# Kernel optimization log

Measured on AMD Instinct MI355X. Metric: run time of the kernel, lower is better.

## Reference

```python
import jax, jax.numpy as jnp
import numpy as np

GROUP_SIZE = 32
PACKED_SIZE = GROUP_SIZE * 3 // 8  # 12
OUT_FEATURES = 4096
IN_FEATURES = 4096

# Precomputed static unpack constants per position i in [0, 32)
_I = np.arange(GROUP_SIZE)
_BYTE_IDX = (_I * 3) // 8                     # which byte holds the low bits
_BIT_OFF = (_I * 3) % 8                       # bit offset inside that byte
_LOW_MASK = np.where(_BIT_OFF <= 5, 7, (1 << (8 - _BIT_OFF)) - 1)
_HIGH_MASK = np.where(_BIT_OFF <= 5, 0, (1 << np.maximum(_BIT_OFF - 5, 0)) - 1)
_HIGH_SHIFT = np.where(_BIT_OFF <= 5, 0, 8 - _BIT_OFF)
_BYTE_IDX_NEXT = np.minimum(_BYTE_IDX + 1, PACKED_SIZE - 1)


def block_dequantize_3bit(packed, normalization):
    """packed: [G, 12] int (uint8 values), normalization: [G, 1] -> [G*32] f32."""
    p = packed.astype(jnp.int32)
    norm = normalization.astype(jnp.float32)
    b0 = p[:, _BYTE_IDX]        # [G, 32]
    b1 = p[:, _BYTE_IDX_NEXT]   # [G, 32]
    shift = jnp.asarray(_BIT_OFF, jnp.int32)
    low = (b0 >> shift) & jnp.asarray(_LOW_MASK, jnp.int32)
    high = (b1 & jnp.asarray(_HIGH_MASK, jnp.int32)) << jnp.asarray(_HIGH_SHIFT, jnp.int32)
    x_quant = (low | high).astype(jnp.float32)  # values in [0, 7]
    x_norm = x_quant / 7.0
    x = x_norm * 2.0 * norm - norm              # [G, 32]
    return x.reshape(-1)


def setup_inputs() -> dict:
    key = jax.random.key(0)
    k1, k2, k3, k4 = jax.random.split(key, 4)
    num_groups = OUT_FEATURES * IN_FEATURES // GROUP_SIZE
    x = jax.random.normal(k1, (8192, IN_FEATURES), dtype=jnp.float32)
    weight_q3 = jax.random.randint(k2, (num_groups, PACKED_SIZE), 0, 256, dtype=jnp.int32).astype(jnp.uint8)
    weight_norm = (jax.random.uniform(k3, (num_groups, 1), dtype=jnp.float32) * 0.99 + 0.01).astype(jnp.float16)
    bias = (jax.random.normal(k4, (OUT_FEATURES,), dtype=jnp.float32) * 0.02).astype(jnp.float16)
    return {"x": x, "weight_q3": weight_q3, "weight_norm": weight_norm, "bias": bias}


def reference(x, weight_q3, weight_norm, bias):
    w_flat = block_dequantize_3bit(weight_q3, weight_norm)          # f32 [out*in]
    w = w_flat.reshape(OUT_FEATURES, IN_FEATURES).astype(jnp.float16)
    x_half = x.astype(jnp.float16)
    result = jnp.dot(x_half, w.T) + bias                             # [N, out] fp16
    return result.astype(x.dtype)
```

## Files before the change

### kernel.cpp

```cpp
#include <hip/hip_runtime.h>
#include <hip/hip_fp16.h>
#include <stdint.h>

#define IN_F   4096
#define OUT_F  4096
#define M_ROWS 8192

typedef _Float16 v8h __attribute__((ext_vector_type(8)));
typedef float    v4f __attribute__((ext_vector_type(4)));

__global__ void __launch_bounds__(256)
prep_kernel(const int* __restrict__ q, const float* __restrict__ norm,
            _Float16* __restrict__ w, const float* __restrict__ x,
            _Float16* __restrict__ xo) {
    int blk = blockIdx.x;
    if (blk < 2048) {
        int g = blk * 256 + threadIdx.x;
        const int4* p = (const int4*)(q + (size_t)g * 12);
        int4 q0 = p[0], q1 = p[1], q2 = p[2];
        uint32_t b[12] = {(uint32_t)q0.x, (uint32_t)q0.y, (uint32_t)q0.z, (uint32_t)q0.w,
                          (uint32_t)q1.x, (uint32_t)q1.y, (uint32_t)q1.z, (uint32_t)q1.w,
                          (uint32_t)q2.x, (uint32_t)q2.y, (uint32_t)q2.z, (uint32_t)q2.w};
        uint64_t lo = 0, hi = 0;
#pragma unroll
        for (int i = 0; i < 8; ++i) lo |= (uint64_t)(b[i] & 0xff) << (8 * i);
#pragma unroll
        for (int i = 0; i < 8; ++i) hi |= (uint64_t)(b[4 + i] & 0xff) << (8 * i);
        float nrm = norm[g];
        float scale = nrm * (2.0f / 7.0f);
        v8h out[4];
#pragma unroll
        for (int i = 0; i < 32; ++i) {
            int p3 = 3 * i;
            uint32_t qv = (i <= 20) ? (uint32_t)((lo >> p3) & 7)
                                    : (uint32_t)((hi >> (p3 - 32)) & 7);
            float v = fmaf((float)qv, scale, -nrm);
            out[i >> 3][i & 7] = (_Float16)v;
        }
        v8h* dst = (v8h*)(w + (size_t)g * 32);
        dst[0] = out[0]; dst[1] = out[1]; dst[2] = out[2]; dst[3] = out[3];
    } else {
        size_t i = ((size_t)(blk - 2048) * 256 + threadIdx.x) * 8;
        float4 a = *(const float4*)(x + i);
        float4 c = *(const float4*)(x + i + 4);
        v8h r;
        r[0] = (_Float16)a.x; r[1] = (_Float16)a.y; r[2] = (_Float16)a.z; r[3] = (_Float16)a.w;
        r[4] = (_Float16)c.x; r[5] = (_Float16)c.y; r[6] = (_Float16)c.z; r[7] = (_Float16)c.w;
        *(v8h*)(xo + i) = r;
    }
}

#define KU 32

__global__ void __launch_bounds__(512, 2)
gemm_kernel(const _Float16* __restrict__ A,
            const _Float16* __restrict__ B,
            const float* __restrict__ bias,
            float* __restrict__ C) {
    __shared__ __align__(16) char smem[131072];

    int pid = blockIdx.x;
    int c  = pid & 7;
    int s  = pid >> 3;
    int pm = ((c & 3) << 3) | (s & 7);
    int pn = ((c >> 2) << 3) | (s >> 3);
    const int m0 = pm * 256, n0 = pn * 256;

    int t = threadIdx.x;
    int lane = t & 63, wid = t >> 6;
    int wm = wid >> 2, wn = wid & 3;
    int lr = lane & 15, qd = lane >> 4;

    int chr  = (((lane & 1) << 2) | qd) ^ ((lr >> 1) & 7);
    int aoff = wm * 8192 + (lr >> 1) * 128 + chr * 16;
    int boff = 16384 + wn * 4096 + (lr >> 1) * 128 + chr * 16;

    int line = t >> 3, chl = t & 7;
    int chd  = chl ^ (line & 7);
    int rr0  = 2 * line + (chd >> 2);
    int cc0  = chd & 3;
    const _Float16* gA0 = A + (size_t)(m0 + rr0) * IN_F + cc0 * 8;
    const _Float16* gA1 = gA0 + (size_t)128 * IN_F;
    const _Float16* gB0 = B + (size_t)(n0 + rr0) * IN_F + cc0 * 8;
    const _Float16* gB1 = gB0 + (size_t)128 * IN_F;
    const int dA = t * 16;
    const int dB = 16384 + t * 16;

    v4f acc[8][4] = {};

#define STAGE4(SL2)                                                                 \
    do {                                                                            \
        char* db_ = smem + (SL2) * 32768;                                           \
        __builtin_amdgcn_global_load_lds(                                           \
            (const __attribute__((address_space(1))) void*)gA0,                     \
            (__attribute__((address_space(3))) void*)(db_ + dA), 16, 0, 0);         \
        __builtin_amdgcn_global_load_lds(                                           \
            (const __attribute__((address_space(1))) void*)gA1,                     \
            (__attribute__((address_space(3))) void*)(db_ + dA + 8192), 16, 0, 0);  \
        __builtin_amdgcn_global_load_lds(                                           \
            (const __attribute__((address_space(1))) void*)gB0,                     \
            (__attribute__((address_space(3))) void*)(db_ + dB), 16, 0, 0);         \
        __builtin_amdgcn_global_load_lds(                                           \
            (const __attribute__((address_space(1))) void*)gB1,                     \
            (__attribute__((address_space(3))) void*)(db_ + dB + 8192), 16, 0, 0);  \
    } while (0)

#define STEP(SL, DO_STAGE, VM)                                                      \
    do {                                                                            \
        asm volatile("" ::: "memory");    \
        const char* slb = smem + (SL) * 32768;                                      \
        v8h a0_[4], a1_[4], bb_[4];                                                 \
        _Pragma("unroll") for (int i = 0; i < 4; ++i)                               \
            a0_[i] = *(const v8h*)(slb + aoff + i * 1024);                          \
        _Pragma("unroll") for (int j = 0; j < 4; ++j)                               \
            bb_[j] = *(const v8h*)(slb + boff + j * 1024);                          \
        _Pragma("unroll") for (int i = 0; i < 4; ++i)                               \
            a1_[i] = *(const v8h*)(slb + aoff + (i + 4) * 1024);                    \
        if (DO_STAGE) {                                                             \
            STAGE4((((SL) + 3) & 3));                                               \
            gA0 += KU; gA1 += KU; gB0 += KU; gB1 += KU;                             \
        }                                                                           \
        __builtin_amdgcn_s_setprio(1);                                              \
        _Pragma("unroll") for (int i = 0; i < 4; ++i)                               \
            _Pragma("unroll") for (int j = 0; j < 4; ++j)                           \
                acc[i][j] = __builtin_amdgcn_mfma_f32_16x16x32_f16(                 \
                    a0_[i], bb_[j], acc[i][j], 0, 0, 0);                            \
        _Pragma("unroll") for (int i = 0; i < 4; ++i)                               \
            _Pragma("unroll") for (int j = 0; j < 4; ++j)                           \
                acc[i + 4][j] = __builtin_amdgcn_mfma_f32_16x16x32_f16(             \
                    a1_[i], bb_[j], acc[i + 4][j], 0, 0, 0);                        \
        __builtin_amdgcn_s_setprio(0);                                              \
        asm volatile("s_waitcnt vmcnt(" #VM ")" ::: "memory");                      \
        __builtin_amdgcn_s_barrier();                                               \
    } while (0)

    STAGE4(0); gA0 += KU; gA1 += KU; gB0 += KU; gB1 += KU;
    STAGE4(1); gA0 += KU; gA1 += KU; gB0 += KU; gB1 += KU;
    STAGE4(2); gA0 += KU; gA1 += KU; gB0 += KU; gB1 += KU;
    asm volatile("s_waitcnt vmcnt(8)" ::: "memory");
    __builtin_amdgcn_s_barrier();

#pragma unroll 1
    for (int b4 = 0; b4 < 31; ++b4) {
        STEP(0, 1, 8);
        STEP(1, 1, 8);
        STEP(2, 1, 8);
        STEP(3, 1, 8);
    }
    STEP(0, 1, 8);
    STEP(1, 0, 4);
    STEP(2, 0, 0);
    STEP(3, 0, 0);
#undef STEP
#undef STAGE4

#pragma unroll
    for (int j = 0; j < 4; ++j) {
        int n = n0 + wn * 64 + j * 16 + lr;
        float bf = bias[n];
#pragma unroll
        for (int i = 0; i < 8; ++i) {
            int m = m0 + wm * 128 + i * 16 + qd * 4;
#pragma unroll
            for (int rr = 0; rr < 4; ++rr)
                C[(size_t)(m + rr) * OUT_F + n] = acc[i][j][rr] + bf;
        }
    }
}

extern "C" void kernel_launch(void* const* d_in, const int* in_sizes, int n_in,
                              void* d_out, int out_size, void* d_ws, size_t ws_size,
                              hipStream_t stream) {
    (void)in_sizes; (void)n_in; (void)out_size; (void)ws_size;
    const float* x    = (const float*)d_in[0];
    const int*   wq   = (const int*)d_in[1];
    const float* wnrm = (const float*)d_in[2];
    const float* bias = (const float*)d_in[3];
    float* out = (float*)d_out;

    _Float16* w16 = (_Float16*)d_ws;
    _Float16* x16 = (_Float16*)((char*)d_ws + (size_t)OUT_F * IN_F * 2);

    prep_kernel<<<2048 + 16384, 256, 0, stream>>>(wq, wnrm, w16, x, x16);

    int grid = (M_ROWS / 256) * (OUT_F / 256);
    gemm_kernel<<<grid, 512, 0, stream>>>(x16, w16, bias, out);
}
```

Before: 499.6 us.

## Double-buffer LDS fragment reads in registers and split prep kernel in two

The GEMM main loop now reads the next k-slice's A/B fragments from LDS into a second register set while MFMAs run on the current set, so LDS read latency overlaps compute. The vmcnt waits are tightened to match the earlier consumption of staged tiles. The fused prep kernel is also split into separate dequant and cast kernels, which adds one launch. The extra 48 fragment registers raise VGPR pressure at 2 waves per SIMD and could force spills.

Result: no change. 499.1 us (-0.1%).

```diff
diff --git a/kernel.cpp b/kernel.cpp
--- a/kernel.cpp
+++ b/kernel.cpp
@@ -10,44 +10,43 @@
 typedef float    v4f __attribute__((ext_vector_type(4)));
 
 __global__ void __launch_bounds__(256)
-prep_kernel(const int* __restrict__ q, const float* __restrict__ norm,
-            _Float16* __restrict__ w, const float* __restrict__ x,
-            _Float16* __restrict__ xo) {
-    int blk = blockIdx.x;
-    if (blk < 2048) {
-        int g = blk * 256 + threadIdx.x;
-        const int4* p = (const int4*)(q + (size_t)g * 12);
-        int4 q0 = p[0], q1 = p[1], q2 = p[2];
-        uint32_t b[12] = {(uint32_t)q0.x, (uint32_t)q0.y, (uint32_t)q0.z, (uint32_t)q0.w,
-                          (uint32_t)q1.x, (uint32_t)q1.y, (uint32_t)q1.z, (uint32_t)q1.w,
-                          (uint32_t)q2.x, (uint32_t)q2.y, (uint32_t)q2.z, (uint32_t)q2.w};
-        uint64_t lo = 0, hi = 0;
+dequant_kernel(const int* __restrict__ q, const float* __restrict__ norm,
+               _Float16* __restrict__ w) {
+    int g = blockIdx.x * blockDim.x + threadIdx.x;
+    const int4* p = (const int4*)(q + (size_t)g * 12);
+    int4 q0 = p[0], q1 = p[1], q2 = p[2];
+    uint32_t b[12] = {(uint32_t)q0.x, (uint32_t)q0.y, (uint32_t)q0.z, (uint32_t)q0.w,
+                      (uint32_t)q1.x, (uint32_t)q1.y, (uint32_t)q1.z, (uint32_t)q1.w,
+                      (uint32_t)q2.x, (uint32_t)q2.y, (uint32_t)q2.z, (uint32_t)q2.w};
+    uint64_t lo = 0, hi = 0;
 #pragma unroll
-        for (int i = 0; i < 8; ++i) lo |= (uint64_t)(b[i] & 0xff) << (8 * i);
+    for (int i = 0; i < 8; ++i) lo |= (uint64_t)(b[i] & 0xff) << (8 * i);
 #pragma unroll
-        for (int i = 0; i < 8; ++i) hi |= (uint64_t)(b[4 + i] & 0xff) << (8 * i);
-        float nrm = norm[g];
-        float scale = nrm * (2.0f / 7.0f);
-        v8h out[4];
+    for (int i = 0; i < 8; ++i) hi |= (uint64_t)(b[4 + i] & 0xff) << (8 * i);
+    float nrm = norm[g];
+    float scale = nrm * (2.0f / 7.0f);
+    v8h out[4];
 #pragma unroll
-        for (int i = 0; i < 32; ++i) {
-            int p3 = 3 * i;
-            uint32_t qv = (i <= 20) ? (uint32_t)((lo >> p3) & 7)
-                                    : (uint32_t)((hi >> (p3 - 32)) & 7);
-            float v = fmaf((float)qv, scale, -nrm);
-            out[i >> 3][i & 7] = (_Float16)v;
-        }
-        v8h* dst = (v8h*)(w + (size_t)g * 32);
-        dst[0] = out[0]; dst[1] = out[1]; dst[2] = out[2]; dst[3] = out[3];
-    } else {
-        size_t i = ((size_t)(blk - 2048) * 256 + threadIdx.x) * 8;
-        float4 a = *(const float4*)(x + i);
-        float4 c = *(const float4*)(x + i + 4);
-        v8h r;
-        r[0] = (_Float16)a.x; r[1] = (_Float16)a.y; r[2] = (_Float16)a.z; r[3] = (_Float16)a.w;
-        r[4] = (_Float16)c.x; r[5] = (_Float16)c.y; r[6] = (_Float16)c.z; r[7] = (_Float16)c.w;
-        *(v8h*)(xo + i) = r;
+    for (int i = 0; i < 32; ++i) {
+        int p3 = 3 * i;
+        uint32_t qv = (i <= 20) ? (uint32_t)((lo >> p3) & 7)
+                                : (uint32_t)((hi >> (p3 - 32)) & 7);
+        float v = fmaf((float)qv, scale, -nrm);
+        out[i >> 3][i & 7] = (_Float16)v;
     }
+    v8h* dst = (v8h*)(w + (size_t)g * 32);
+    dst[0] = out[0]; dst[1] = out[1]; dst[2] = out[2]; dst[3] = out[3];
+}
+
+__global__ void __launch_bounds__(256)
+castx_kernel(const float* __restrict__ x, _Float16* __restrict__ o) {
+    size_t i = ((size_t)blockIdx.x * blockDim.x + threadIdx.x) * 8;
+    float4 a = *(const float4*)(x + i);
+    float4 b = *(const float4*)(x + i + 4);
+    v8h r;
+    r[0] = (_Float16)a.x; r[1] = (_Float16)a.y; r[2] = (_Float16)a.z; r[3] = (_Float16)a.w;
+    r[4] = (_Float16)b.x; r[5] = (_Float16)b.y; r[6] = (_Float16)b.z; r[7] = (_Float16)b.w;
+    *(v8h*)(o + i) = r;
 }
 
 #define KU 32
@@ -87,6 +86,7 @@
     const int dB = 16384 + t * 16;
 
     v4f acc[8][4] = {};
+    v8h fa0[8], fb0[4], fa1[8], fb1[4];
 
 #define STAGE4(SL2)                                                                 \
     do {                                                                            \
@@ -105,30 +105,28 @@
             (__attribute__((address_space(3))) void*)(db_ + dB + 8192), 16, 0, 0);  \
     } while (0)
 
-#define STEP(SL, DO_STAGE, VM)                                                      \
+#define READFRAG(SLOT, FA, FB)                                                      \
     do {                                                                            \
-        asm volatile("" ::: "memory");    \
-        const char* slb = smem + (SL) * 32768;                                      \
-        v8h a0_[4], a1_[4], bb_[4];                                                 \
-        _Pragma("unroll") for (int i = 0; i < 4; ++i)                               \
-            a0_[i] = *(const v8h*)(slb + aoff + i * 1024);                          \
+        const char* sp_ = smem + (SLOT) * 32768;                                    \
+        _Pragma("unroll") for (int i = 0; i < 8; ++i)                               \
+            FA[i] = *(const v8h*)(sp_ + aoff + i * 1024);                           \
         _Pragma("unroll") for (int j = 0; j < 4; ++j)                               \
-            bb_[j] = *(const v8h*)(slb + boff + j * 1024);                          \
-        _Pragma("unroll") for (int i = 0; i < 4; ++i)                               \
-            a1_[i] = *(const v8h*)(slb + aoff + (i + 4) * 1024);                    \
+            FB[j] = *(const v8h*)(sp_ + boff + j * 1024);                           \
+    } while (0)
+
+#define STEP(SL, FCA, FCB, FNA, FNB, DO_STAGE, DO_PREF, VM)                         \
+    do {                                                                            \
+        asm volatile("" ::: "memory");      \
+        if (DO_PREF) READFRAG(((SL) + 1) & 3, FNA, FNB);                            \
         if (DO_STAGE) {                                                             \
-            STAGE4((((SL) + 3) & 3));                                               \
+            STAGE4(((SL) + 3) & 3);                                                 \
             gA0 += KU; gA1 += KU; gB0 += KU; gB1 += KU;                             \
         }                                                                           \
         __builtin_amdgcn_s_setprio(1);                                              \
-        _Pragma("unroll") for (int i = 0; i < 4; ++i)                               \
+        _Pragma("unroll") for (int i = 0; i < 8; ++i)                               \
             _Pragma("unroll") for (int j = 0; j < 4; ++j)                           \
                 acc[i][j] = __builtin_amdgcn_mfma_f32_16x16x32_f16(                 \
-                    a0_[i], bb_[j], acc[i][j], 0, 0, 0);                            \
-        _Pragma("unroll") for (int i = 0; i < 4; ++i)                               \
-            _Pragma("unroll") for (int j = 0; j < 4; ++j)                           \
-                acc[i + 4][j] = __builtin_amdgcn_mfma_f32_16x16x32_f16(             \
-                    a1_[i], bb_[j], acc[i + 4][j], 0, 0, 0);                        \
+                    FCA[i], FCB[j], acc[i][j], 0, 0, 0);                            \
         __builtin_amdgcn_s_setprio(0);                                              \
         asm volatile("s_waitcnt vmcnt(" #VM ")" ::: "memory");                      \
         __builtin_amdgcn_s_barrier();                                               \
@@ -137,21 +135,24 @@
     STAGE4(0); gA0 += KU; gA1 += KU; gB0 += KU; gB1 += KU;
     STAGE4(1); gA0 += KU; gA1 += KU; gB0 += KU; gB1 += KU;
     STAGE4(2); gA0 += KU; gA1 += KU; gB0 += KU; gB1 += KU;
-    asm volatile("s_waitcnt vmcnt(8)" ::: "memory");
+    asm volatile("s_waitcnt vmcnt(4)" ::: "memory");
     __builtin_amdgcn_s_barrier();
+    asm volatile("" ::: "memory");
+    READFRAG(0, fa0, fb0);
 
 #pragma unroll 1
     for (int b4 = 0; b4 < 31; ++b4) {
-        STEP(0, 1, 8);
-        STEP(1, 1, 8);
-        STEP(2, 1, 8);
-        STEP(3, 1, 8);
+        STEP(0, fa0, fb0, fa1, fb1, 1, 1, 4);
+        STEP(1, fa1, fb1, fa0, fb0, 1, 1, 4);
+        STEP(2, fa0, fb0, fa1, fb1, 1, 1, 4);
+        STEP(3, fa1, fb1, fa0, fb0, 1, 1, 4);
     }
-    STEP(0, 1, 8);
-    STEP(1, 0, 4);
-    STEP(2, 0, 0);
-    STEP(3, 0, 0);
+    STEP(0, fa0, fb0, fa1, fb1, 1, 1, 4);
+    STEP(1, fa1, fb1, fa0, fb0, 0, 1, 0);
+    STEP(2, fa0, fb0, fa1, fb1, 0, 1, 0);
+    STEP(3, fa1, fb1, fa0, fb0, 0, 0, 0);
 #undef STEP
+#undef READFRAG
 #undef STAGE4
 
 #pragma unroll
@@ -181,7 +182,9 @@
     _Float16* w16 = (_Float16*)d_ws;
     _Float16* x16 = (_Float16*)((char*)d_ws + (size_t)OUT_F * IN_F * 2);
 
-    prep_kernel<<<2048 + 16384, 256, 0, stream>>>(wq, wnrm, w16, x, x16);
+    const int NUM_GROUPS = OUT_F * IN_F / 32;
+    dequant_kernel<<<NUM_GROUPS / 256, 256, 0, stream>>>(wq, wnrm, w16);
+    castx_kernel<<<(size_t)M_ROWS * IN_F / 8 / 256, 256, 0, stream>>>(x, x16);
 
     int grid = (M_ROWS / 256) * (OUT_F / 256);
     gemm_kernel<<<grid, 512, 0, stream>>>(x16, w16, bias, out);
```
